# Optimization experiments

Hardware: AMD Instinct MI355X
Metric: run time of the kernel (lower is better)

Reference implementation:

```python
import jax, jax.numpy as jnp
import numpy as np

B, T, N, E = 8, 16, 2048, 32768
F_IN, C, EDGE_DIM = 32, 32, 1


def setup_inputs() -> dict:
    key = jax.random.key(0)
    ks = jax.random.split(key, 12)
    s = 1.0 / np.sqrt(C)
    x = jax.random.normal(ks[0], (B, T, N, F_IN), jnp.float32)
    edge_index = jax.random.randint(ks[1], (2, E), 0, N)
    edge_attr = jax.random.normal(ks[2], (E, EDGE_DIM), jnp.float32)
    Wl = jax.random.normal(ks[3], (F_IN, C), jnp.float32) * s
    bl = jnp.zeros((C,), jnp.float32)
    Wr = jax.random.normal(ks[4], (F_IN, C), jnp.float32) * s
    br = jnp.zeros((C,), jnp.float32)
    We = jax.random.normal(ks[5], (EDGE_DIM, C), jnp.float32) * s
    att = jax.random.normal(ks[6], (C,), jnp.float32) * s
    out_bias = jnp.zeros((C,), jnp.float32)
    w_ih = jax.random.normal(ks[7], (3 * C, C), jnp.float32) * s
    w_hh = jax.random.normal(ks[8], (3 * C, C), jnp.float32) * s
    b_ih = jnp.zeros((3 * C,), jnp.float32)
    b_hh = jnp.zeros((3 * C,), jnp.float32)
    return dict(x=x, edge_index=edge_index, edge_attr=edge_attr, Wl=Wl, bl=bl,
                Wr=Wr, br=br, We=We, att=att, out_bias=out_bias,
                w_ih=w_ih, w_hh=w_hh, b_ih=b_ih, b_hh=b_hh)


def _gatv2(x, edge_index, edge_attr, Wl, bl, Wr, br, We, att, out_bias):
    # x: [B,T,N,F]; GATv2Conv, heads=1, negative_slope=0.2, self loops w/ mean edge attr
    n = x.shape[2]
    src, dst = edge_index[0], edge_index[1]
    deg = jax.ops.segment_sum(jnp.ones((src.shape[0],), x.dtype), dst, num_segments=n)
    mean_attr = jax.ops.segment_sum(edge_attr, dst, num_segments=n) / jnp.maximum(deg, 1.0)[:, None]
    loop = jnp.arange(n)
    src_a = jnp.concatenate([src, loop])
    dst_a = jnp.concatenate([dst, loop])
    attr_a = jnp.concatenate([edge_attr, mean_attr], axis=0)
    xl = x @ Wl + bl  # [B,T,N,C]
    xr = x @ Wr + br
    e_emb = attr_a @ We  # [E2,C]
    xls = jnp.take(xl, src_a, axis=2)  # [B,T,E2,C]
    m = jax.nn.leaky_relu(xls + jnp.take(xr, dst_a, axis=2) + e_emb, 0.2)
    s = jnp.einsum('btec,c->ebt', m, att)  # [E2,B,T]
    smax = jax.ops.segment_max(s, dst_a, num_segments=n)
    es = jnp.exp(s - smax[dst_a])
    denom = jax.ops.segment_sum(es, dst_a, num_segments=n)
    alpha = es / denom[dst_a]  # segment softmax over incoming edges, [E2,B,T]
    msg = xls * alpha.transpose(1, 2, 0)[..., None]  # [B,T,E2,C]
    out = jax.ops.segment_sum(msg.transpose(2, 0, 1, 3), dst_a, num_segments=n)
    return out.transpose(1, 2, 0, 3) + out_bias  # [B,T,N,C]


def _gru(seq, w_ih, w_hh, b_ih, b_hh):
    # seq: [BN, T, C]; torch GRU gate order r,z,n
    c = seq.shape[-1]

    def step(h, xt):
        gi = xt @ w_ih.T + b_ih
        gh = h @ w_hh.T + b_hh
        ir, iz, inn = jnp.split(gi, 3, axis=-1)
        hr, hz, hn = jnp.split(gh, 3, axis=-1)
        r = jax.nn.sigmoid(ir + hr)
        z = jax.nn.sigmoid(iz + hz)
        nc = jnp.tanh(inn + r * hn)
        h = (1.0 - z) * nc + z * h
        return h, h

    h0 = jnp.zeros((seq.shape[0], c), seq.dtype)
    _, ys = jax.lax.scan(step, h0, seq.transpose(1, 0, 2))
    return ys.transpose(1, 0, 2)


def reference(x, edge_index, edge_attr, Wl, bl, Wr, br, We, att, out_bias, w_ih, w_hh, b_ih, b_hh):
    b, t, n, _ = x.shape
    h = _gatv2(x, edge_index, edge_attr, Wl, bl, Wr, br, We, att, out_bias)
    seq = h.transpose(0, 2, 1, 3).reshape(b * n, t, -1)
    y = _gru(seq, w_ih, w_hh, b_ih, b_hh)
    return y.reshape(b, n, t, -1).transpose(0, 2, 1, 3)
```

## Files before the change

### kernel.cpp

```cpp
#include <hip/hip_runtime.h>
#include <hip/hip_bf16.h>

#define N_NODES 2048
#define N_EDGES 32768
#define BT      128
#define TT      16
#define CH      32
#define E2      (N_EDGES + N_NODES)

static __device__ __forceinline__ unsigned pk2(float a, float b) {
    __hip_bfloat162 h2(__float2bfloat16(a), __float2bfloat16(b));
    return *reinterpret_cast<unsigned*>(&h2);
}

__global__ void deg_attr_kernel(const int* __restrict__ ei,
                                const float* __restrict__ ea,
                                int* __restrict__ deg, float* __restrict__ asum) {
    int e = blockIdx.x * 256 + threadIdx.x;
    if (e < N_EDGES) {
        int dst = ei[N_EDGES + e];
        atomicAdd(&deg[dst], 1);
        atomicAdd(&asum[dst], ea[e]);
    }
}

__global__ void scan_kernel(const int* __restrict__ deg, int* __restrict__ rowp) {
    int lane = threadIdx.x;
    int base = lane * 32;
    int loc[32];
    int s = 0;
    #pragma unroll
    for (int i = 0; i < 32; ++i) { loc[i] = s; s += deg[base + i] + 1; }
    int inc = s;
    #pragma unroll
    for (int d = 1; d < 64; d <<= 1) {
        int v = __shfl_up(inc, d, 64);
        if (lane >= d) inc += v;
    }
    int excl = inc - s;
    #pragma unroll
    for (int i = 0; i < 32; ++i) rowp[base + i] = excl + loc[i];
    if (lane == 63) rowp[N_NODES] = inc;
}

__global__ void scatter_kernel(const int* __restrict__ ei,
                               const float* __restrict__ ea,
                               const int* __restrict__ deg, const float* __restrict__ asum,
                               const int* __restrict__ rowp, int* __restrict__ fill,
                               int* __restrict__ col, float* __restrict__ attr_s) {
    int e = blockIdx.x * 256 + threadIdx.x;
    if (e >= E2) return;
    int src, dst; float a;
    if (e < N_EDGES) {
        src = ei[e]; dst = ei[N_EDGES + e]; a = ea[e];
    } else {
        int n = e - N_EDGES;
        src = n; dst = n;
        a = asum[n] / fmaxf((float)deg[n], 1.0f);
    }
    int pos = atomicAdd(&fill[dst], 1);
    col[rowp[dst] + pos]    = src;
    attr_s[rowp[dst] + pos] = a;
}

__global__ __launch_bounds__(256) void proj_kernel(
        const float* __restrict__ x,
        const float* __restrict__ Wl, const float* __restrict__ bl,
        const float* __restrict__ Wr, const float* __restrict__ br,
        unsigned* __restrict__ xlt, unsigned* __restrict__ xrt) {
    __shared__ float xs[128 * 32];
    __shared__ float wl[1024], wr[1024];
    int n = blockIdx.x;
    int tid = threadIdx.x;
    for (int i = tid; i < 1024; i += 256) { wl[i] = Wl[i]; wr[i] = Wr[i]; }
    #pragma unroll
    for (int i = 0; i < 16; ++i) {
        int e = i * 256 + tid;
        int bt = e >> 5, f = e & 31;
        xs[e] = x[((long)bt * N_NODES + n) * 32 + f];
    }
    __syncthreads();
    int c2  = tid & 15;
    int btl = tid >> 4;
    int c0 = 2 * c2, c1 = c0 + 1;
    float bl0 = bl[c0], bl1 = bl[c1];
    float br0 = br[c0], br1 = br[c1];
    for (int i = 0; i < 8; ++i) {
        int bt = i * 16 + btl;
        float a0 = 0.f, a1 = 0.f, r0 = 0.f, r1 = 0.f;
        #pragma unroll
        for (int f = 0; f < 32; ++f) {
            float xv = xs[bt * 32 + f];
            a0 = fmaf(xv, wl[f * 32 + c0], a0);
            a1 = fmaf(xv, wl[f * 32 + c1], a1);
            r0 = fmaf(xv, wr[f * 32 + c0], r0);
            r1 = fmaf(xv, wr[f * 32 + c1], r1);
        }
        long o = (long)n * 2048 + c2 * 128 + bt;
        xlt[o] = pk2(a0 + bl0, a1 + bl1);
        xrt[o] = pk2(r0 + br0, r1 + br1);
    }
}

__global__ __launch_bounds__(64) void gat_kernel(
        const unsigned* __restrict__ xlt,
        const unsigned* __restrict__ xrt,
        const int* __restrict__ rowp, const int* __restrict__ col,
        const float* __restrict__ attr_s,
        const float* __restrict__ We, const float* __restrict__ att,
        const float* __restrict__ ob,
        const float* __restrict__ wih, const float* __restrict__ bih,
        __hip_bfloat16* __restrict__ gi) {
    int lane = threadIdx.x;
    int task = blockIdx.x;
    int n   = task >> 1;
    int bt  = ((task & 1) << 6) | lane;

    float xrv[32];
    {
        const unsigned* rp = xrt + (long)n * 2048 + bt;
        #pragma unroll
        for (int c2 = 0; c2 < 16; ++c2) {
            unsigned u = rp[c2 * 128];
            xrv[2*c2]   = __uint_as_float(u << 16);
            xrv[2*c2+1] = __uint_as_float(u & 0xffff0000u);
        }
    }

    float accv[32];
    #pragma unroll
    for (int c = 0; c < 32; ++c) accv[c] = 0.f;

    int beg = rowp[n];
    int end = rowp[n + 1];
    float den = 0.f;
    const unsigned* xbase = xlt + bt;
    for (int j = beg; j < end; ++j) {
        int   src = col[j];
        float av  = attr_s[j];
        const unsigned* gp = xbase + (long)src * 2048;
        unsigned u[16];
        #pragma unroll
        for (int c2 = 0; c2 < 16; ++c2) u[c2] = gp[c2 * 128];

        float p0 = 0.f, p1 = 0.f, p2 = 0.f, p3 = 0.f;
        #pragma unroll
        for (int c2 = 0; c2 < 16; ++c2) {
            unsigned w2 = u[c2];
            float x0 = __uint_as_float(w2 << 16);
            float x1 = __uint_as_float(w2 & 0xffff0000u);
            int c = 2 * c2;
            float m0 = x0 + fmaf(av, We[c],     xrv[c]);
            float m1 = x1 + fmaf(av, We[c + 1], xrv[c + 1]);
            if (c2 & 1) { p2 = fmaf(att[c], fmaxf(m0, 0.2f * m0), p2);
                          p3 = fmaf(att[c + 1], fmaxf(m1, 0.2f * m1), p3); }
            else        { p0 = fmaf(att[c], fmaxf(m0, 0.2f * m0), p0);
                          p1 = fmaf(att[c + 1], fmaxf(m1, 0.2f * m1), p1); }
        }
        float p = fminf((p0 + p1) + (p2 + p3), 80.f);
        float w = __expf(p);
        den += w;
        #pragma unroll
        for (int c2 = 0; c2 < 16; ++c2) {
            unsigned w2 = u[c2];
            accv[2*c2]   = fmaf(w, __uint_as_float(w2 << 16),         accv[2*c2]);
            accv[2*c2+1] = fmaf(w, __uint_as_float(w2 & 0xffff0000u), accv[2*c2+1]);
        }
    }
    float inv = 1.f / den;
    #pragma unroll
    for (int c = 0; c < 32; ++c) accv[c] = fmaf(accv[c], inv, ob[c]);

    __hip_bfloat16* gip = gi + ((long)bt * N_NODES + n) * 96;
    #pragma unroll
    for (int g8 = 0; g8 < 12; ++g8) {
        float s0 = bih[g8*8+0], s1 = bih[g8*8+1], s2 = bih[g8*8+2], s3 = bih[g8*8+3];
        float s4 = bih[g8*8+4], s5 = bih[g8*8+5], s6 = bih[g8*8+6], s7 = bih[g8*8+7];
        #pragma unroll
        for (int f = 0; f < 32; ++f) {
            float hf = accv[f];
            s0 = fmaf(hf, wih[(g8*8+0)*32+f], s0);
            s1 = fmaf(hf, wih[(g8*8+1)*32+f], s1);
            s2 = fmaf(hf, wih[(g8*8+2)*32+f], s2);
            s3 = fmaf(hf, wih[(g8*8+3)*32+f], s3);
            s4 = fmaf(hf, wih[(g8*8+4)*32+f], s4);
            s5 = fmaf(hf, wih[(g8*8+5)*32+f], s5);
            s6 = fmaf(hf, wih[(g8*8+6)*32+f], s6);
            s7 = fmaf(hf, wih[(g8*8+7)*32+f], s7);
        }
        uint4 v;
        v.x = pk2(s0, s1); v.y = pk2(s2, s3); v.z = pk2(s4, s5); v.w = pk2(s6, s7);
        *(uint4*)(gip + g8 * 8) = v;
    }
}

__global__ __launch_bounds__(256) void gru_kernel(
        const float* __restrict__ whh, const float* __restrict__ bhh,
        const __hip_bfloat16* __restrict__ gi,
        float* __restrict__ out) {
    int tid  = threadIdx.x;
    int lane = tid & 63;
    int c    = lane & 31;
    int half = lane >> 5;
    int fbase = half << 4;
    int seq  = blockIdx.x * 4 + (tid >> 6);
    int b = seq >> 11;
    int n = seq & 2047;

    float w0[16], w1[16], w2[16];
    #pragma unroll
    for (int k4 = 0; k4 < 4; ++k4) {
        float4 a0 = *(const float4*)&whh[( 0 + c) * 32 + fbase + k4 * 4];
        float4 a1 = *(const float4*)&whh[(32 + c) * 32 + fbase + k4 * 4];
        float4 a2 = *(const float4*)&whh[(64 + c) * 32 + fbase + k4 * 4];
        w0[k4*4+0]=a0.x; w0[k4*4+1]=a0.y; w0[k4*4+2]=a0.z; w0[k4*4+3]=a0.w;
        w1[k4*4+0]=a1.x; w1[k4*4+1]=a1.y; w1[k4*4+2]=a1.z; w1[k4*4+3]=a1.w;
        w2[k4*4+0]=a2.x; w2[k4*4+1]=a2.y; w2[k4*4+2]=a2.z; w2[k4*4+3]=a2.w;
    }
    float bh0 = half ? 0.f : bhh[c];
    float bh1 = half ? 0.f : bhh[32 + c];
    float bh2 = half ? 0.f : bhh[64 + c];

    const long GSTR = (long)N_NODES * 96;
    long gbase = ((long)b * TT * N_NODES + n) * 96 + c;
    const long OSTR = (long)N_NODES * CH;
    long obase = ((long)b * TT * N_NODES + n) * CH + c;

    float hc = 0.f;
    float gr = __bfloat162float(gi[gbase]);
    float gz = __bfloat162float(gi[gbase + 32]);
    float gn = __bfloat162float(gi[gbase + 64]);
    #pragma unroll 1
    for (int t = 0; t < TT; ++t) {
        long gnx = gbase + (long)(t + 1) * GSTR;
        float grn = 0.f, gzn = 0.f, gnn = 0.f;
        if (t + 1 < TT) {
            grn = __bfloat162float(gi[gnx]);
            gzn = __bfloat162float(gi[gnx + 32]);
            gnn = __bfloat162float(gi[gnx + 64]);
        }
        float g0 = bh0, g1 = bh1, g2 = bh2;
        #pragma unroll
        for (int k = 0; k < 16; ++k) {
            float v = __shfl(hc, fbase + k, 64);
            g0 = fmaf(v, w0[k], g0);
            g1 = fmaf(v, w1[k], g1);
            g2 = fmaf(v, w2[k], g2);
        }
        float G0 = g0 + __shfl_xor(g0, 32, 64);
        float G1 = g1 + __shfl_xor(g1, 32, 64);
        float G2 = g2 + __shfl_xor(g2, 32, 64);
        float r  = 1.f / (1.f + __expf(-(gr + G0)));
        float z  = 1.f / (1.f + __expf(-(gz + G1)));
        float a  = fmaf(r, G2, gn);
        float e2 = __expf(2.f * a);
        float nc = 1.f - 2.f / (e2 + 1.f);
        hc = (1.f - z) * nc + z * hc;
        if (half == 0) out[obase + (long)t * OSTR] = hc;
        gr = grn; gz = gzn; gn = gnn;
    }
}

extern "C" void kernel_launch(void* const* d_in, const int* in_sizes, int n_in,
                              void* d_out, int out_size, void* d_ws, size_t ws_size,
                              hipStream_t stream) {
    const float* x    = (const float*)d_in[0];
    const int*   ei   = (const int*)d_in[1];
    const float* ea   = (const float*)d_in[2];
    const float* Wl   = (const float*)d_in[3];
    const float* bl   = (const float*)d_in[4];
    const float* Wr   = (const float*)d_in[5];
    const float* br   = (const float*)d_in[6];
    const float* We   = (const float*)d_in[7];
    const float* att  = (const float*)d_in[8];
    const float* ob   = (const float*)d_in[9];
    const float* wih  = (const float*)d_in[10];
    const float* whh  = (const float*)d_in[11];
    const float* bih  = (const float*)d_in[12];
    const float* bhh  = (const float*)d_in[13];
    float* out = (float*)d_out;

    int*   deg  = (int*)d_ws;
    float* asum = (float*)(deg + N_NODES);
    int*   fill = (int*)(asum + N_NODES);
    int*   rowp = fill + N_NODES;
    int*   col  = rowp + (N_NODES + 16);
    float* attr_s = (float*)(col + E2);
    unsigned* xlt = (unsigned*)(attr_s + E2);
    xlt = (unsigned*)(((uintptr_t)xlt + 255) & ~(uintptr_t)255);
    unsigned* xrt = xlt + (long)N_NODES * 2048;
    __hip_bfloat16* gi = (__hip_bfloat16*)(xrt + (long)N_NODES * 2048);

    hipMemsetAsync(deg, 0, 3 * N_NODES * sizeof(int), stream);

    deg_attr_kernel<<<N_EDGES / 256, 256, 0, stream>>>(ei, ea, deg, asum);
    scan_kernel<<<1, 64, 0, stream>>>(deg, rowp);
    scatter_kernel<<<(E2 + 255) / 256, 256, 0, stream>>>(ei, ea, deg, asum, rowp, fill, col, attr_s);
    proj_kernel<<<N_NODES, 256, 0, stream>>>(x, Wl, bl, Wr, br, xlt, xrt);
    gat_kernel<<<N_NODES * 2, 64, 0, stream>>>(xlt, xrt, rowp, col, attr_s,
                                               We, att, ob, wih, bih, gi);
    gru_kernel<<<(BT / TT * N_NODES) / 4, 256, 0, stream>>>(whh, bhh, gi, out);
}
```

Measured before the change: 251.8 us.

## Repack projected features into 16-byte channel groups for vectorized gathers

Changes the xl/xr intermediate layout so that, for each node, eight bf16 channels per batch-time slot are stored contiguously as a uint4. The GAT edge loop then gathers each source node with four 16-byte loads instead of sixteen 4-byte loads. The projection kernel is reorganized so each thread computes 16 channels for one bt slot, with padded shared memory to avoid bank conflicts. This raises register use in the projection kernel in exchange for fewer, wider memory transactions in the gather-heavy GAT kernel.

```diff
diff --git a/kernel.cpp b/kernel.cpp
--- a/kernel.cpp
+++ b/kernel.cpp
@@ -67,8 +67,8 @@
         const float* __restrict__ x,
         const float* __restrict__ Wl, const float* __restrict__ bl,
         const float* __restrict__ Wr, const float* __restrict__ br,
-        unsigned* __restrict__ xlt, unsigned* __restrict__ xrt) {
-    __shared__ float xs[128 * 32];
+        uint4* __restrict__ xlt4, uint4* __restrict__ xrt4) {
+    __shared__ float xs[128 * 33];
     __shared__ float wl[1024], wr[1024];
     int n = blockIdx.x;
     int tid = threadIdx.x;
@@ -77,34 +77,46 @@
     for (int i = 0; i < 16; ++i) {
         int e = i * 256 + tid;
         int bt = e >> 5, f = e & 31;
-        xs[e] = x[((long)bt * N_NODES + n) * 32 + f];
+        xs[bt * 33 + f] = x[((long)bt * N_NODES + n) * 32 + f];
     }
     __syncthreads();
-    int c2  = tid & 15;
-    int btl = tid >> 4;
-    int c0 = 2 * c2, c1 = c0 + 1;
-    float bl0 = bl[c0], bl1 = bl[c1];
-    float br0 = br[c0], br1 = br[c1];
-    for (int i = 0; i < 8; ++i) {
-        int bt = i * 16 + btl;
-        float a0 = 0.f, a1 = 0.f, r0 = 0.f, r1 = 0.f;
+    int bt    = tid & 127;
+    int chalf = tid >> 7;
+    int cbase = chalf << 4;
+    float xf[32];
+    #pragma unroll
+    for (int f = 0; f < 32; ++f) xf[f] = xs[bt * 33 + f];
+    float av[16], rv[16];
+    #pragma unroll
+    for (int c = 0; c < 16; ++c) {
+        float a = 0.f, r = 0.f;
         #pragma unroll
         for (int f = 0; f < 32; ++f) {
-            float xv = xs[bt * 32 + f];
-            a0 = fmaf(xv, wl[f * 32 + c0], a0);
-            a1 = fmaf(xv, wl[f * 32 + c1], a1);
-            r0 = fmaf(xv, wr[f * 32 + c0], r0);
-            r1 = fmaf(xv, wr[f * 32 + c1], r1);
-        }
-        long o = (long)n * 2048 + c2 * 128 + bt;
-        xlt[o] = pk2(a0 + bl0, a1 + bl1);
-        xrt[o] = pk2(r0 + br0, r1 + br1);
-    }
+            a = fmaf(xf[f], wl[f * 32 + cbase + c], a);
+            r = fmaf(xf[f], wr[f * 32 + cbase + c], r);
+        }
+        av[c] = a + bl[cbase + c];
+        rv[c] = r + br[cbase + c];
+    }
+    long base = (long)n * 512 + (chalf * 2) * 128 + bt;
+    uint4 v;
+    v.x = pk2(av[0], av[1]);  v.y = pk2(av[2], av[3]);
+    v.z = pk2(av[4], av[5]);  v.w = pk2(av[6], av[7]);
+    xlt4[base] = v;
+    v.x = pk2(av[8], av[9]);  v.y = pk2(av[10], av[11]);
+    v.z = pk2(av[12], av[13]); v.w = pk2(av[14], av[15]);
+    xlt4[base + 128] = v;
+    v.x = pk2(rv[0], rv[1]);  v.y = pk2(rv[2], rv[3]);
+    v.z = pk2(rv[4], rv[5]);  v.w = pk2(rv[6], rv[7]);
+    xrt4[base] = v;
+    v.x = pk2(rv[8], rv[9]);  v.y = pk2(rv[10], rv[11]);
+    v.z = pk2(rv[12], rv[13]); v.w = pk2(rv[14], rv[15]);
+    xrt4[base + 128] = v;
 }
 
 __global__ __launch_bounds__(64) void gat_kernel(
-        const unsigned* __restrict__ xlt,
-        const unsigned* __restrict__ xrt,
+        const uint4* __restrict__ xlt4,
+        const uint4* __restrict__ xrt4,
         const int* __restrict__ rowp, const int* __restrict__ col,
         const float* __restrict__ attr_s,
         const float* __restrict__ We, const float* __restrict__ att,
@@ -118,12 +130,14 @@
 
     float xrv[32];
     {
-        const unsigned* rp = xrt + (long)n * 2048 + bt;
+        const uint4* rp = xrt4 + (long)n * 512 + bt;
+        uint4 R0 = rp[0], R1 = rp[128], R2 = rp[256], R3 = rp[384];
+        unsigned u[16] = {R0.x,R0.y,R0.z,R0.w, R1.x,R1.y,R1.z,R1.w,
+                          R2.x,R2.y,R2.z,R2.w, R3.x,R3.y,R3.z,R3.w};
         #pragma unroll
         for (int c2 = 0; c2 < 16; ++c2) {
-            unsigned u = rp[c2 * 128];
-            xrv[2*c2]   = __uint_as_float(u << 16);
-            xrv[2*c2+1] = __uint_as_float(u & 0xffff0000u);
+            xrv[2*c2]   = __uint_as_float(u[c2] << 16);
+            xrv[2*c2+1] = __uint_as_float(u[c2] & 0xffff0000u);
         }
     }
 
@@ -134,14 +148,14 @@
     int beg = rowp[n];
     int end = rowp[n + 1];
     float den = 0.f;
-    const unsigned* xbase = xlt + bt;
+    const uint4* xbase = xlt4 + bt;
     for (int j = beg; j < end; ++j) {
         int   src = col[j];
         float av  = attr_s[j];
-        const unsigned* gp = xbase + (long)src * 2048;
-        unsigned u[16];
-        #pragma unroll
-        for (int c2 = 0; c2 < 16; ++c2) u[c2] = gp[c2 * 128];
+        const uint4* gp = xbase + (long)src * 512;
+        uint4 U0 = gp[0], U1 = gp[128], U2 = gp[256], U3 = gp[384];
+        unsigned u[16] = {U0.x,U0.y,U0.z,U0.w, U1.x,U1.y,U1.z,U1.w,
+                          U2.x,U2.y,U2.z,U2.w, U3.x,U3.y,U3.z,U3.w};
 
         float p0 = 0.f, p1 = 0.f, p2 = 0.f, p3 = 0.f;
         #pragma unroll
@@ -296,8 +310,10 @@
     deg_attr_kernel<<<N_EDGES / 256, 256, 0, stream>>>(ei, ea, deg, asum);
     scan_kernel<<<1, 64, 0, stream>>>(deg, rowp);
     scatter_kernel<<<(E2 + 255) / 256, 256, 0, stream>>>(ei, ea, deg, asum, rowp, fill, col, attr_s);
-    proj_kernel<<<N_NODES, 256, 0, stream>>>(x, Wl, bl, Wr, br, xlt, xrt);
-    gat_kernel<<<N_NODES * 2, 64, 0, stream>>>(xlt, xrt, rowp, col, attr_s,
+    proj_kernel<<<N_NODES, 256, 0, stream>>>(x, Wl, bl, Wr, br,
+                                             (uint4*)xlt, (uint4*)xrt);
+    gat_kernel<<<N_NODES * 2, 64, 0, stream>>>((const uint4*)xlt, (const uint4*)xrt,
+                                               rowp, col, attr_s,
                                                We, att, ob, wih, bih, gi);
     gru_kernel<<<(BT / TT * N_NODES) / 4, 256, 0, stream>>>(whh, bhh, gi, out);
 }
```

After: 237.4 us. -5.7%, faster.
